# Performance work log

Measured on AMD Instinct MI355X. Metric: run time of the kernel, lower is better.

## Reference

```python
import jax, jax.numpy as jnp
import numpy as np

B, R, P, DP, DR, N, RK = 4, 256, 64, 384, 512, 48, 24


def _ln(x, w, b, eps=1e-5):
    m = x.mean(-1, keepdims=True)
    v = ((x - m) ** 2).mean(-1, keepdims=True)
    return (x - m) / jnp.sqrt(v + eps) * w + b


def _l2norm(x, eps=1e-6):
    return x / jnp.maximum(jnp.linalg.norm(x, axis=-1, keepdims=True), eps)


def setup_inputs() -> dict:
    key = jax.random.key(0)
    ks = jax.random.split(key, 16)
    s = 0.02
    rnd = lambda k, shp: jax.random.normal(k, shp, jnp.float32) * s
    inp = {
        'patch_tokens': jax.random.normal(ks[0], (B, R, P, DP), jnp.float32),
        'patch_mask': jax.random.randint(ks[1], (B, R, P), 0, 2) > 0,
        'near_mask': jax.random.randint(ks[2], (R, R), 0, 2) > 0,
        'far_mask': jax.random.randint(ks[3], (R, R), 0, 2) > 0,
        'local_pos': rnd(ks[4], (1, 1, P, DP)),
        'gate_ln_w': jnp.ones(DP), 'gate_ln_b': jnp.zeros(DP),
        'gate_w1': rnd(ks[5], (DP, DR)), 'gate_b1': jnp.zeros(DR),
        'gate_w2': rnd(ks[6], (DR, 1)), 'gate_b2': jnp.zeros(1),
        'proj_ln1_w': jnp.ones(DP), 'proj_ln1_b': jnp.zeros(DP),
        'proj_w1': rnd(ks[7], (DP, DR)), 'proj_b1': jnp.zeros(DR),
        'proj_w2': rnd(ks[8], (DR, DR)), 'proj_b2': jnp.zeros(DR),
        'proj_ln2_w': jnp.ones(DR), 'proj_ln2_b': jnp.zeros(DR),
        'in_proj_w': rnd(ks[9], (DR, 2 * DR)),
        'x_proj_w': rnd(ks[10], (DR, RK + 2 * N)),
        'dt_w': rnd(ks[11], (RK, DR)),
        'dt_b': jax.random.uniform(ks[12], (DR,), jnp.float32, -4.0, -2.0),
        'A_log': jnp.tile(jnp.log(jnp.arange(1, N + 1, dtype=jnp.float32))[None, :], (DR, 1)),
        'D_param': jnp.ones(DR),
        'out_proj_w': rnd(ks[13], (DR, DR)),
        'scan_ln_w': jnp.ones(DR), 'scan_ln_b': jnp.zeros(DR),
    }
    return inp


def _forward(patch_tokens, patch_mask, near_mask, far_mask, local_pos,
             gate_ln_w, gate_ln_b, gate_w1, gate_b1, gate_w2, gate_b2,
             proj_ln1_w, proj_ln1_b, proj_w1, proj_b1, proj_w2, proj_b2,
             proj_ln2_w, proj_ln2_b, in_proj_w, x_proj_w, dt_w, dt_b,
             A_log, D_param, out_proj_w, scan_ln_w, scan_ln_b):
    # ---- GatedRegionAggregator ----
    x = patch_tokens + local_pos  # [B,R,P,DP]
    g = _ln(x, gate_ln_w, gate_ln_b)
    g = jax.nn.gelu(g @ gate_w1 + gate_b1, approximate=False)
    logits = (g @ gate_w2 + gate_b2)[..., 0]  # [B,R,P]
    logits = jnp.where(patch_mask, logits, jnp.finfo(logits.dtype).min)
    attn = jax.nn.softmax(logits, axis=-1) * patch_mask
    attn = attn / jnp.maximum(attn.sum(-1, keepdims=True), 1e-6)
    pooled = jnp.einsum('brp,brpd->brd', attn, x)  # [B,R,DP]
    p = _ln(pooled, proj_ln1_w, proj_ln1_b)
    p = jax.nn.gelu(p @ proj_w1 + proj_b1, approximate=False)
    p = _ln(p @ proj_w2 + proj_b2, proj_ln2_w, proj_ln2_b)
    p = jnp.nan_to_num(p, nan=0.0, posinf=1.0, neginf=-1.0)
    region = _l2norm(p)  # [B,R,DR]

    # ---- SlowSelectiveScan1D over region sequence (L = R) ----
    xz = region @ in_proj_w  # [B,L,2*DR]
    u, z = jnp.split(xz, 2, axis=-1)
    prm = u @ x_proj_w  # [B,L,RK+2N]
    dt_raw, Bm, Cm = prm[..., :RK], prm[..., RK:RK + N], prm[..., RK + N:]
    delta = jnp.minimum(jax.nn.softplus(dt_raw @ dt_w + dt_b), 10.0)  # [B,L,DR]
    A = -jnp.minimum(jnp.exp(A_log), 1e4)  # [DR,N]
    dA = jnp.exp(jnp.clip(delta[..., None] * A[None, None], -30.0, 30.0))  # [B,L,DR,N]
    dBu = delta[..., None] * Bm[:, :, None, :] * u[..., None]  # [B,L,DR,N]
    log_cumA = jnp.cumsum(jnp.log(jnp.maximum(dA, 1e-38)), axis=1)
    h = jnp.exp(log_cumA) * jnp.cumsum(dBu * jnp.exp(-log_cumA), axis=1)
    y_seq = jnp.einsum('bln,bldn->bld', Cm, h) + D_param * u
    y = (y_seq * jax.nn.silu(z)) @ out_proj_w
    out = _ln(region + jnp.nan_to_num(y, nan=0.0, posinf=1.0, neginf=-1.0),
              scan_ln_w, scan_ln_b)  # [B,R,DR]

    # ---- topology_loss_static ----
    rt = _l2norm(out.astype(jnp.float32))
    sim = jnp.einsum('brd,bsd->brs', rt, rt)  # [B,R,R]
    near = near_mask.astype(sim.dtype)[None]
    far = far_mask.astype(sim.dtype)[None]
    near_loss = ((1.0 - sim) * near).sum() / jnp.maximum(near.sum(), 1.0)
    far_loss = (jax.nn.relu(sim - 0.2) * far).sum() / jnp.maximum(far.sum(), 1.0)
    return out, near_loss + far_loss


def reference(patch_tokens, patch_mask, near_mask, far_mask, local_pos,
              gate_ln_w, gate_ln_b, gate_w1, gate_b1, gate_w2, gate_b2,
              proj_ln1_w, proj_ln1_b, proj_w1, proj_b1, proj_w2, proj_b2,
              proj_ln2_w, proj_ln2_b, in_proj_w, x_proj_w, dt_w, dt_b,
              A_log, D_param, out_proj_w, scan_ln_w, scan_ln_b):
    return _forward(patch_tokens, patch_mask, near_mask, far_mask, local_pos,
                    gate_ln_w, gate_ln_b, gate_w1, gate_b1, gate_w2, gate_b2,
                    proj_ln1_w, proj_ln1_b, proj_w1, proj_b1, proj_w2, proj_b2,
                    proj_ln2_w, proj_ln2_b, in_proj_w, x_proj_w, dt_w, dt_b,
                    A_log, D_param, out_proj_w, scan_ln_w, scan_ln_b)
```

## Files before the change

### kernel.cpp

```cpp
#include <hip/hip_runtime.h>
#include <hip/hip_bf16.h>
#include <math.h>

#define B_ 4
#define R_ 256
#define P_ 64
#define DP_ 384
#define DR_ 512
#define N_ 48
#define RK_ 24
#define MROWS (B_*R_*P_)
#define REGS  (B_*R_)

typedef unsigned short ushort_t;
typedef __attribute__((ext_vector_type(8))) short bf16x8;
typedef __attribute__((ext_vector_type(4))) float f32x4;

#define GLOAD16(g, l) __builtin_amdgcn_global_load_lds( \
    (const __attribute__((address_space(1))) unsigned int*)(g), \
    (__attribute__((address_space(3))) unsigned int*)(l), 16, 0, 0)

#define OFF_PW1  0
#define OFF_PW2  196608
#define OFF_INPW 458752
#define OFF_XPW  983040
#define OFF_DTW  1044480
#define NW_TOT   1056768

__device__ __forceinline__ float us2f(unsigned short u){
  union { unsigned int i; float f; } x; x.i = ((unsigned int)u) << 16; return x.f;
}
__device__ __forceinline__ unsigned short f2us(float f){
  __hip_bfloat16 h = __float2bfloat16(f);
  return *reinterpret_cast<unsigned short*>(&h);
}
__device__ __forceinline__ float gelu_f(float x){
  return 0.5f * x * (1.0f + erff(x * 0.70710678118654752f));
}
__device__ __forceinline__ float wred_sum(float v){
#pragma unroll
  for (int m = 1; m < 64; m <<= 1) v += __shfl_xor(v, m, 64);
  return v;
}
__device__ __forceinline__ void block_sum4(float v[4], float* s){
  int lane = threadIdx.x & 63, wid = threadIdx.x >> 6;
#pragma unroll
  for (int i = 0; i < 4; ++i){
    float x = v[i];
#pragma unroll
    for (int m = 1; m < 64; m <<= 1) x += __shfl_xor(x, m, 64);
    if (lane == 0) s[wid * 4 + i] = x;
  }
  __syncthreads();
  if (threadIdx.x < 4){
    float t = 0.f;
    for (int t2 = 0; t2 < 8; ++t2) t += s[t2 * 4 + threadIdx.x];
    s[32 + threadIdx.x] = t;
  }
  __syncthreads();
#pragma unroll
  for (int i = 0; i < 4; ++i) v[i] = s[32 + i];
  __syncthreads();
}
__device__ __forceinline__ void block_sum2(float& a, float& b, float* s){
  int lane = threadIdx.x & 63, wid = threadIdx.x >> 6;
  float x = a, y = b;
#pragma unroll
  for (int m = 1; m < 64; m <<= 1){ x += __shfl_xor(x, m, 64); y += __shfl_xor(y, m, 64); }
  if (lane == 0){ s[wid * 2] = x; s[wid * 2 + 1] = y; }
  __syncthreads();
  if (threadIdx.x < 2){
    float t = 0.f;
    for (int j = 0; j < 8; ++j) t += s[j * 2 + threadIdx.x];
    s[16 + threadIdx.x] = t;
  }
  __syncthreads();
  a = s[16]; b = s[17];
  __syncthreads();
}

__global__ __launch_bounds__(512) void k_prep(
    const float* __restrict__ gw1, const float* __restrict__ glnw,
    const float* __restrict__ glnb, const float* __restrict__ gb1,
    ushort_t* __restrict__ W1pT, float* __restrict__ s1,
    float* __restrict__ b1p, float* __restrict__ accum){
  __shared__ float pss[8][64], psb[8][64];
  int tid = threadIdx.x, seg = tid >> 6, nl = tid & 63;
  int n = blockIdx.x * 64 + nl;
  if (blockIdx.x == 0 && tid < 4) accum[tid] = 0.f;
  float s = 0.f, sb = 0.f;
  int k0 = seg * 48;
  for (int i = 0; i < 48; ++i){
    int k = k0 + i;
    float w1 = gw1[k * DR_ + n];
    float v = glnw[k] * w1;
    unsigned short vr = f2us(v);
    s  += us2f(vr);
    sb += glnb[k] * w1;
    W1pT[(size_t)n * DP_ + k] = vr;
  }
  pss[seg][nl] = s; psb[seg][nl] = sb;
  __syncthreads();
  if (tid < 64){
    float ts = 0.f, tb = 0.f;
    for (int j = 0; j < 8; ++j){ ts += pss[j][tid]; tb += psb[j][tid]; }
    s1[blockIdx.x * 64 + tid] = ts;
    b1p[blockIdx.x * 64 + tid] = gb1[blockIdx.x * 64 + tid] + tb;
  }
}

__global__ __launch_bounds__(512) void k_cast(
    const float* __restrict__ pw1, const float* __restrict__ pw2,
    const float* __restrict__ inpw, const float* __restrict__ xpw,
    const float* __restrict__ dtw, ushort_t* __restrict__ dst){
  int i = (blockIdx.x * 512 + threadIdx.x) * 4;
  if (i >= NW_TOT) return;
  const float* s; int off;
  if (i < OFF_PW2){ s = pw1; off = OFF_PW1; }
  else if (i < OFF_INPW){ s = pw2; off = OFF_PW2; }
  else if (i < OFF_XPW){ s = inpw; off = OFF_INPW; }
  else if (i < OFF_DTW){ s = xpw; off = OFF_XPW; }
  else { s = dtw; off = OFF_DTW; }
  float4 v = *(const float4*)(s + (i - off));
  ushort_t* d = dst + i;
  d[0] = f2us(v.x); d[1] = f2us(v.y); d[2] = f2us(v.z); d[3] = f2us(v.w);
}

__global__ __launch_bounds__(512) void k_xform(
    const float* __restrict__ pt, const float* __restrict__ lp,
    ushort_t* __restrict__ xb, float* __restrict__ mu, float* __restrict__ rsg){
  int tid = threadIdx.x, w = tid >> 6, lane = tid & 63;
  size_t r = (size_t)blockIdx.x * 8 + w;
  int p = (int)(r & (P_ - 1));
  const float* xr = pt + r * DP_ + lane * 6;
  const float* lr = lp + (size_t)p * DP_ + lane * 6;
  float x[6];
  float s = 0.f, ss = 0.f;
#pragma unroll
  for (int i = 0; i < 6; i += 2){
    float2 a = *(const float2*)(xr + i);
    float2 b = *(const float2*)(lr + i);
    x[i] = a.x + b.x; x[i + 1] = a.y + b.y;
  }
#pragma unroll
  for (int i = 0; i < 6; ++i){ s += x[i]; ss += x[i] * x[i]; }
  s = wred_sum(s); ss = wred_sum(ss);
  if (lane == 0){
    float m = s * (1.f / DP_);
    float var = ss * (1.f / DP_) - m * m;
    mu[r] = m;
    rsg[r] = rsqrtf(var + 1e-5f);
  }
  ushort_t* xw = xb + r * DP_ + lane * 6;
#pragma unroll
  for (int i = 0; i < 6; i += 2){
    ushort2 u2; u2.x = f2us(x[i]); u2.y = f2us(x[i + 1]);
    *(ushort2*)(xw + i) = u2;
  }
}

__global__ __launch_bounds__(512, 4) void k_gate_pool(
    const ushort_t* __restrict__ xb,
    const ushort_t* __restrict__ BT,
    const float* __restrict__ mu, const float* __restrict__ rsg,
    const float* __restrict__ s1, const float* __restrict__ b1p,
    const float* __restrict__ w2, const int* __restrict__ pmask,
    float* __restrict__ pooled){
  __shared__ __align__(16) ushort_t Abuf[2][64 * 64];
  __shared__ float logit_lds[64];
  __shared__ float smu[64], srs[64];
  __shared__ float attn[64];
  int tid = threadIdx.x;
  int lane = tid & 63, w = tid >> 6;
  int t = lane & 15, g = lane >> 4;
  long r0 = (long)blockIdx.x * 64;
  if (tid < 64){
    logit_lds[tid] = 0.f;
    smu[tid] = mu[r0 + tid];
    srs[tid] = rsg[r0 + tid];
  }

  f32x4 acc[4][4];
#pragma unroll
  for (int m = 0; m < 4; ++m)
#pragma unroll
    for (int n = 0; n < 4; ++n) acc[m][n] = (f32x4){0.f, 0.f, 0.f, 0.f};

  int arow8 = (w << 3) + (lane >> 3);
  int akc = lane & 7;
  const ushort_t* asrc0 = xb + (size_t)(r0 + arow8) * DP_ + ((akc ^ (arow8 & 7)) << 3);
  ushort_t* adst0 = Abuf[0] + (w << 9);
  ushort_t* adst1 = Abuf[1] + (w << 9);

  GLOAD16(asrc0, adst0);
  __syncthreads();

  for (int kt = 0; kt < 6; ++kt){
    if (kt < 5) GLOAD16(asrc0 + (kt + 1) * 64, (kt & 1) ? adst0 : adst1);
    const ushort_t* cbuf = (kt & 1) ? Abuf[1] : Abuf[0];
    bf16x8 bfr[2][4];
#pragma unroll
    for (int kk = 0; kk < 2; ++kk)
#pragma unroll
      for (int n = 0; n < 4; ++n){
        int rowb = w * 64 + n * 16 + t;
        bfr[kk][n] = *(const bf16x8*)(BT + (size_t)rowb * DP_ + kt * 64 + (kk * 4 + g) * 8);
      }
#pragma unroll
    for (int kk = 0; kk < 2; ++kk){
      int ch = kk * 4 + g;
      bf16x8 af[4];
#pragma unroll
      for (int m = 0; m < 4; ++m){
        int row = m * 16 + t;
        af[m] = *(const bf16x8*)(cbuf + row * 64 + ((ch ^ (row & 7)) << 3));
      }
#pragma unroll
      for (int m = 0; m < 4; ++m)
#pragma unroll
        for (int n = 0; n < 4; ++n)
          acc[m][n] = __builtin_amdgcn_mfma_f32_16x16x32_bf16(af[m], bfr[kk][n], acc[m][n], 0, 0, 0);
    }
    __syncthreads();
  }

  float w2c[4], s1c[4], b1c[4];
#pragma unroll
  for (int n = 0; n < 4; ++n){
    int c = w * 64 + n * 16 + t;
    w2c[n] = w2[c]; s1c[n] = s1[c]; b1c[n] = b1p[c];
  }
#pragma unroll
  for (int m = 0; m < 4; ++m){
#pragma unroll
    for (int j = 0; j < 4; ++j){
      int rl = m * 16 + g * 4 + j;
      float mur = smu[rl], rs = srs[rl];
      float part = 0.f;
#pragma unroll
      for (int n = 0; n < 4; ++n){
        float gp = rs * acc[m][n][j] - mur * rs * s1c[n] + b1c[n];
        part += gelu_f(gp) * w2c[n];
      }
#pragma unroll
      for (int msk = 1; msk < 16; msk <<= 1) part += __shfl_xor(part, msk, 64);
      if (t == 0) atomicAdd(&logit_lds[rl], part);
    }
  }
  __syncthreads();

  if (tid < 64){
    int mk = pmask[r0 + tid];
    float lv = logit_lds[tid];
    float lm = mk ? lv : -3.4e38f;
    float M = lm;
#pragma unroll
    for (int m2 = 1; m2 < 64; m2 <<= 1) M = fmaxf(M, __shfl_xor(M, m2, 64));
    float e = mk ? __expf(lv - M) : 0.f;
    float S = e;
#pragma unroll
    for (int m2 = 1; m2 < 64; m2 <<= 1) S += __shfl_xor(S, m2, 64);
    float a = (S > 0.f) ? e / S : 0.f;
    float S2 = a;
#pragma unroll
    for (int m2 = 1; m2 < 64; m2 <<= 1) S2 += __shfl_xor(S2, m2, 64);
    attn[tid] = a / fmaxf(S2, 1e-6f);
  }
  __syncthreads();

  if (tid < DP_){
    float accp = 0.f;
#pragma unroll 4
    for (int p = 0; p < P_; ++p)
      accp += attn[p] * us2f(xb[(size_t)(r0 + p) * DP_ + tid]);
    pooled[(long)blockIdx.x * DP_ + tid] = accp;
  }
}

__global__ __launch_bounds__(512, 4) void k_region(
    const float* __restrict__ pooled,
    const float* __restrict__ ln1w, const float* __restrict__ ln1b,
    const ushort_t* __restrict__ wblob, const float* __restrict__ pb1,
    const float* __restrict__ pb2,
    const float* __restrict__ ln2w, const float* __restrict__ ln2b,
    const float* __restrict__ dtb,
    float* __restrict__ region, float* __restrict__ uT, float* __restrict__ zT,
    float* __restrict__ deltaT, float* __restrict__ BmT, float* __restrict__ CmT){
  const ushort_t* pw1b  = wblob + OFF_PW1;
  const ushort_t* pw2b  = wblob + OFF_PW2;
  const ushort_t* inpwb = wblob + OFF_INPW;
  const ushort_t* xpwb  = wblob + OFF_XPW;
  const ushort_t* dtwb  = wblob + OFF_DTW;
  __shared__ float xr[2][DP_];
  __shared__ float p1[2][DR_];
  __shared__ float rg[2][DR_];
  __shared__ float us[2][DR_];
  __shared__ float ps[4][2][128];
  __shared__ float prm[2][RK_ + 2 * N_];
  __shared__ float red[24];
  int tid = threadIdx.x;
  int r0 = blockIdx.x * 2;
  for (int i = tid; i < 2 * DP_; i += 512) xr[i / DP_][i % DP_] = pooled[(long)r0 * DP_ + i];
  __syncthreads();
  float v0 = (tid < DP_) ? xr[0][tid] : 0.f;
  float v1 = (tid < DP_) ? xr[1][tid] : 0.f;
  float s0 = v0, s1v = v1;
  block_sum2(s0, s1v, red);
  float dv0 = (tid < DP_) ? (v0 - s0 * (1.f / DP_)) : 0.f;
  float dv1 = (tid < DP_) ? (v1 - s1v * (1.f / DP_)) : 0.f;
  float q0 = dv0 * dv0, q1 = dv1 * dv1;
  block_sum2(q0, q1, red);
  if (tid < DP_){
    float lw = ln1w[tid], lb = ln1b[tid];
    xr[0][tid] = dv0 * rsqrtf(q0 * (1.f / DP_) + 1e-5f) * lw + lb;
    xr[1][tid] = dv1 * rsqrtf(q1 * (1.f / DP_) + 1e-5f) * lw + lb;
  }
  __syncthreads();
  {
    float pb = pb1[tid];
    float a0 = pb, a1 = pb;
    for (int k0 = 0; k0 < DP_; k0 += 16){
      ushort_t wv[16];
#pragma unroll
      for (int j = 0; j < 16; ++j) wv[j] = pw1b[(k0 + j) * DR_ + tid];
#pragma unroll
      for (int j = 0; j < 16; ++j){
        float wf = us2f(wv[j]);
        a0 = fmaf(xr[0][k0 + j], wf, a0);
        a1 = fmaf(xr[1][k0 + j], wf, a1);
      }
    }
    p1[0][tid] = gelu_f(a0); p1[1][tid] = gelu_f(a1);
  }
  __syncthreads();
  float qq0, qq1;
  {
    float pb = pb2[tid];
    float a0 = pb, a1 = pb;
    for (int k0 = 0; k0 < DR_; k0 += 16){
      ushort_t wv[16];
#pragma unroll
      for (int j = 0; j < 16; ++j) wv[j] = pw2b[(k0 + j) * DR_ + tid];
#pragma unroll
      for (int j = 0; j < 16; ++j){
        float wf = us2f(wv[j]);
        a0 = fmaf(p1[0][k0 + j], wf, a0);
        a1 = fmaf(p1[1][k0 + j], wf, a1);
      }
    }
    qq0 = a0; qq1 = a1;
  }
  {
    float m0 = qq0, m1 = qq1;
    block_sum2(m0, m1, red);
    float d0 = qq0 - m0 * (1.f / DR_), d1 = qq1 - m1 * (1.f / DR_);
    float w0 = d0 * d0, w1 = d1 * d1;
    block_sum2(w0, w1, red);
    float lw = ln2w[tid], lb = ln2b[tid];
    float o0 = d0 * rsqrtf(w0 * (1.f / DR_) + 1e-5f) * lw + lb;
    float o1 = d1 * rsqrtf(w1 * (1.f / DR_) + 1e-5f) * lw + lb;
    if (isnan(o0)) o0 = 0.f; else if (isinf(o0)) o0 = (o0 > 0.f) ? 1.f : -1.f;
    if (isnan(o1)) o1 = 0.f; else if (isinf(o1)) o1 = (o1 > 0.f) ? 1.f : -1.f;
    float n0 = o0 * o0, n1 = o1 * o1;
    block_sum2(n0, n1, red);
    float r0v = o0 / fmaxf(sqrtf(n0), 1e-6f);
    float r1v = o1 / fmaxf(sqrtf(n1), 1e-6f);
    rg[0][tid] = r0v; rg[1][tid] = r1v;
    region[(long)r0 * DR_ + tid] = r0v;
    region[(long)(r0 + 1) * DR_ + tid] = r1v;
  }
  __syncthreads();
  {
    float ua0 = 0.f, ua1 = 0.f, zb0 = 0.f, zb1 = 0.f;
    for (int k0 = 0; k0 < DR_; k0 += 8){
      ushort_t w1v[8], w2v[8];
#pragma unroll
      for (int j = 0; j < 8; ++j){
        w1v[j] = inpwb[(k0 + j) * 1024 + tid];
        w2v[j] = inpwb[(k0 + j) * 1024 + tid + 512];
      }
#pragma unroll
      for (int j = 0; j < 8; ++j){
        float x0 = rg[0][k0 + j], x1 = rg[1][k0 + j];
        float wa = us2f(w1v[j]), wb = us2f(w2v[j]);
        ua0 = fmaf(x0, wa, ua0); ua1 = fmaf(x1, wa, ua1);
        zb0 = fmaf(x0, wb, zb0); zb1 = fmaf(x1, wb, zb1);
      }
    }
    us[0][tid] = ua0; us[1][tid] = ua1;
    uT[(long)tid * REGS + r0] = ua0;
    uT[(long)tid * REGS + r0 + 1] = ua1;
    zT[(long)tid * REGS + r0] = zb0;
    zT[(long)tid * REGS + r0 + 1] = zb1;
  }
  __syncthreads();
  {
    int sseg = tid >> 7, c = tid & 127;
    float pr0 = 0.f, pr1 = 0.f;
    if (c < RK_ + 2 * N_){
      int kb = sseg * 128;
      for (int k0 = kb; k0 < kb + 128; k0 += 16){
        ushort_t wv[16];
#pragma unroll
        for (int j = 0; j < 16; ++j) wv[j] = xpwb[(k0 + j) * (RK_ + 2 * N_) + c];
#pragma unroll
        for (int j = 0; j < 16; ++j){
          float wf = us2f(wv[j]);
          pr0 = fmaf(us[0][k0 + j], wf, pr0);
          pr1 = fmaf(us[1][k0 + j], wf, pr1);
        }
      }
    }
    ps[sseg][0][c] = pr0; ps[sseg][1][c] = pr1;
  }
  __syncthreads();
  if (tid < 256){
    int rr2 = tid >> 7, cc = tid & 127;
    if (cc < RK_ + 2 * N_)
      prm[rr2][cc] = ps[0][rr2][cc] + ps[1][rr2][cc] + ps[2][rr2][cc] + ps[3][rr2][cc];
  }
  __syncthreads();
#pragma unroll
  for (int r = 0; r < 2; ++r){
    float aa = dtb[tid];
#pragma unroll
    for (int j = 0; j < RK_; ++j) aa = fmaf(prm[r][j], us2f(dtwb[j * DR_ + tid]), aa);
    float sp = (aa > 20.f) ? aa : log1pf(expf(aa));
    deltaT[(long)tid * REGS + r0 + r] = fminf(sp, 10.f);
  }
  if (tid < N_){
#pragma unroll
    for (int r = 0; r < 2; ++r){
      BmT[(long)tid * REGS + r0 + r] = prm[r][RK_ + tid];
      CmT[(long)tid * REGS + r0 + r] = prm[r][RK_ + N_ + tid];
    }
  }
}

__global__ __launch_bounds__(256) void k_scan(
    const float* __restrict__ deltaT, const float* __restrict__ uT,
    const float* __restrict__ zT, const float* __restrict__ BmT,
    const float* __restrict__ CmT, const float* __restrict__ alog,
    const float* __restrict__ Dp, float* __restrict__ ys){
  __shared__ float sAn[N_];
  __shared__ float sA[N_][4];
  __shared__ float sB[N_][4];
  int tid = threadIdx.x, lane = tid & 63, w = tid >> 6;
  int ch = blockIdx.x;
  int b = ch >> 9, d = ch & (DR_ - 1);
  if (tid < N_) sAn[tid] = -fminf(__expf(alog[d * N_ + tid]), 10000.f);
  long col = (long)b * R_ + tid;
  float dl = deltaT[(long)d * REGS + col];
  float uu = uT[(long)d * REGS + col];
  float zz = zT[(long)d * REGS + col];
  float Dd = Dp[d];
  float part = 0.f;
  __syncthreads();
  for (int nc = 0; nc < 6; ++nc){
    float bmv[8], cmv[8];
#pragma unroll
    for (int j = 0; j < 8; ++j){
      bmv[j] = BmT[(long)(nc * 8 + j) * REGS + col];
      cmv[j] = CmT[(long)(nc * 8 + j) * REGS + col];
    }
    float aA[8], aB[8];
#pragma unroll
    for (int j = 0; j < 8; ++j){
      int n = nc * 8 + j;
      float cc = fminf(fmaxf(dl * sAn[n], -30.f), 30.f);
      float a = exp2f(cc * 1.44269504f);
      float bv = dl * bmv[j] * uu;
#pragma unroll
      for (int s = 1; s < 64; s <<= 1){
        float a_sh = __shfl_up(a, (unsigned)s, 64);
        float b_sh = __shfl_up(bv, (unsigned)s, 64);
        float nb = fmaf(a, b_sh, bv);
        float na = a * a_sh;
        if (lane >= s){ bv = nb; a = na; }
      }
      aA[j] = a; aB[j] = bv;
      if (lane == 63){ sA[n][w] = a; sB[n][w] = bv; }
    }
    __syncthreads();
#pragma unroll
    for (int j = 0; j < 8; ++j){
      int n = nc * 8 + j;
      float hin = 0.f;
#pragma unroll
      for (int tt = 0; tt < 3; ++tt){
        if (tt < w) hin = sA[n][tt] * hin + sB[n][tt];
      }
      float h = fmaf(aA[j], hin, aB[j]);
      part = fmaf(cmv[j], h, part);
    }
    if (nc < 5) __syncthreads();
  }
  float yv = part + Dd * uu;
  float sz = zz / (1.f + __expf(-zz));
  ys[col * DR_ + d] = yv * sz;
}

__global__ __launch_bounds__(512) void k_out(
    const float* __restrict__ ys, const float* __restrict__ W,
    const float* __restrict__ region, const float* __restrict__ lnw,
    const float* __restrict__ lnb, float* __restrict__ outp,
    float* __restrict__ rt){
  __shared__ float yr[4][DR_];
  __shared__ float red[40];
  int tid = threadIdx.x;
  int r0 = blockIdx.x * 4;
  for (int i = tid; i < 4 * DR_; i += 512) yr[i >> 9][i & 511] = ys[(long)r0 * DR_ + i];
  __syncthreads();
  float y[4] = {0,0,0,0};
  for (int k0 = 0; k0 < DR_; k0 += 8){
    float wv[8];
#pragma unroll
    for (int j = 0; j < 8; ++j) wv[j] = W[(k0 + j) * DR_ + tid];
#pragma unroll
    for (int j = 0; j < 8; ++j){
#pragma unroll
      for (int i = 0; i < 4; ++i) y[i] = fmaf(yr[i][k0 + j], wv[j], y[i]);
    }
  }
  float v[4], t4[4];
#pragma unroll
  for (int i = 0; i < 4; ++i){
    if (isnan(y[i])) y[i] = 0.f; else if (isinf(y[i])) y[i] = (y[i] > 0.f) ? 1.f : -1.f;
    v[i] = region[(long)(r0 + i) * DR_ + tid] + y[i];
    t4[i] = v[i];
  }
  block_sum4(t4, red);
  float dv[4];
#pragma unroll
  for (int i = 0; i < 4; ++i){ dv[i] = v[i] - t4[i] * (1.f / DR_); t4[i] = dv[i] * dv[i]; }
  block_sum4(t4, red);
  float o[4];
  float lw = lnw[tid], lb = lnb[tid];
#pragma unroll
  for (int i = 0; i < 4; ++i){
    o[i] = dv[i] * rsqrtf(t4[i] * (1.f / DR_) + 1e-5f) * lw + lb;
    outp[(long)(r0 + i) * DR_ + tid] = o[i];
    t4[i] = o[i] * o[i];
  }
  block_sum4(t4, red);
#pragma unroll
  for (int i = 0; i < 4; ++i)
    rt[(long)(r0 + i) * DR_ + tid] = o[i] / fmaxf(sqrtf(t4[i]), 1e-6f);
}

__global__ __launch_bounds__(512) void k_loss(
    const float* __restrict__ rt, const int* __restrict__ nearm,
    const int* __restrict__ farm, float* __restrict__ accum){
  __shared__ __align__(16) float ar[4][DR_];
  __shared__ float ps[2][4][256];
  __shared__ float wsum[8][4];
  int blk = blockIdx.x, tid = threadIdx.x;
  int b = blk >> 6, q0 = (blk & 63) * 4;
  const float* rtb = rt + (long)b * R_ * DR_;
  for (int i = tid; i < 4 * DR_; i += 512) ar[i >> 9][i & 511] = rtb[(long)q0 * DR_ + i];
  __syncthreads();
  int s = tid & 255, h = tid >> 8;
  const float* rsrow = rtb + (long)s * DR_ + h * 256;
  float dq[4] = {0.f, 0.f, 0.f, 0.f};
  for (int k = 0; k < 256; k += 4){
    float4 yv = *(const float4*)(rsrow + k);
#pragma unroll
    for (int q = 0; q < 4; ++q){
      float4 x = *(const float4*)(&ar[q][h * 256 + k]);
      dq[q] += x.x * yv.x + x.y * yv.y + x.z * yv.z + x.w * yv.w;
    }
  }
#pragma unroll
  for (int q = 0; q < 4; ++q) ps[h][q][s] = dq[q];
  __syncthreads();
  float nl = 0.f, fl = 0.f, nc = 0.f, fc = 0.f;
  if (tid < 256){
#pragma unroll
    for (int q = 0; q < 4; ++q){
      float dot = ps[0][q][tid] + ps[1][q][tid];
      int nm = nearm[(q0 + q) * R_ + tid], fm = farm[(q0 + q) * R_ + tid];
      if (nm){ nl += 1.f - dot; if (b == 0) nc += 1.f; }
      if (fm){ fl += fmaxf(dot - 0.2f, 0.f); if (b == 0) fc += 1.f; }
    }
  }
  nl = wred_sum(nl); fl = wred_sum(fl); nc = wred_sum(nc); fc = wred_sum(fc);
  int w = tid >> 6, lane = tid & 63;
  if (lane == 0){ wsum[w][0] = nl; wsum[w][1] = fl; wsum[w][2] = nc; wsum[w][3] = fc; }
  __syncthreads();
  if (tid == 0){
    float a0 = 0, a1 = 0, a2 = 0, a3 = 0;
    for (int i = 0; i < 8; i++){ a0 += wsum[i][0]; a1 += wsum[i][1]; a2 += wsum[i][2]; a3 += wsum[i][3]; }
    atomicAdd(&accum[0], a0); atomicAdd(&accum[1], a1);
    if (b == 0){ atomicAdd(&accum[2], a2); atomicAdd(&accum[3], a3); }
  }
}

__global__ void k_final(const float* __restrict__ accum, float* __restrict__ outp){
  if (threadIdx.x == 0){
    float loss = accum[0] / fmaxf(accum[2], 1.f) + accum[1] / fmaxf(accum[3], 1.f);
    outp[REGS * DR_] = loss;
  }
}

extern "C" void kernel_launch(void* const* d_in, const int* in_sizes, int n_in,
                              void* d_out, int out_size, void* d_ws, size_t ws_size,
                              hipStream_t stream){
  const float* pt    = (const float*)d_in[0];
  const int*   pmask = (const int*)d_in[1];
  const int*   nearm = (const int*)d_in[2];
  const int*   farm  = (const int*)d_in[3];
  const float* lp    = (const float*)d_in[4];
  const float* glnw  = (const float*)d_in[5];
  const float* glnb  = (const float*)d_in[6];
  const float* gw1   = (const float*)d_in[7];
  const float* gb1   = (const float*)d_in[8];
  const float* gw2   = (const float*)d_in[9];
  const float* pln1w = (const float*)d_in[11];
  const float* pln1b = (const float*)d_in[12];
  const float* pw1   = (const float*)d_in[13];
  const float* pb1   = (const float*)d_in[14];
  const float* pw2   = (const float*)d_in[15];
  const float* pb2   = (const float*)d_in[16];
  const float* pln2w = (const float*)d_in[17];
  const float* pln2b = (const float*)d_in[18];
  const float* inpw  = (const float*)d_in[19];
  const float* xpw   = (const float*)d_in[20];
  const float* dtw   = (const float*)d_in[21];
  const float* dtb   = (const float*)d_in[22];
  const float* alog  = (const float*)d_in[23];
  const float* dpar  = (const float*)d_in[24];
  const float* opw   = (const float*)d_in[25];
  const float* slnw  = (const float*)d_in[26];
  const float* slnb  = (const float*)d_in[27];

  char* ws = (char*)d_ws;
  size_t off = 0;
  auto alloc = [&](size_t bytes){ size_t o = off; off += (bytes + 255) & ~(size_t)255; return o; };
  ushort_t* W1pT  = (ushort_t*)(ws + alloc((size_t)DR_ * DP_ * 2));
  float* s1     = (float*)(ws + alloc(DR_ * 4));
  float* b1p    = (float*)(ws + alloc(DR_ * 4));
  ushort_t* wblob = (ushort_t*)(ws + alloc((size_t)NW_TOT * 2));
  ushort_t* xb  = (ushort_t*)(ws + alloc((size_t)MROWS * DP_ * 2));
  float* mu     = (float*)(ws + alloc((size_t)MROWS * 4));
  float* rsg    = (float*)(ws + alloc((size_t)MROWS * 4));
  float* pooled = (float*)(ws + alloc((size_t)REGS * DP_ * 4));
  float* region = (float*)(ws + alloc((size_t)REGS * DR_ * 4));
  float* uT     = (float*)(ws + alloc((size_t)REGS * DR_ * 4));
  float* zT     = (float*)(ws + alloc((size_t)REGS * DR_ * 4));
  float* deltaT = (float*)(ws + alloc((size_t)REGS * DR_ * 4));
  float* BmT    = (float*)(ws + alloc((size_t)REGS * N_ * 4));
  float* CmT    = (float*)(ws + alloc((size_t)REGS * N_ * 4));
  float* ys     = (float*)(ws + alloc((size_t)REGS * DR_ * 4));
  float* rt     = (float*)(ws + alloc((size_t)REGS * DR_ * 4));
  float* accum  = (float*)(ws + alloc(4 * 4));

  float* outp = (float*)d_out;

  k_prep<<<dim3(8), dim3(512), 0, stream>>>(gw1, glnw, glnb, gb1, W1pT, s1, b1p, accum);
  k_cast<<<dim3((NW_TOT / 4 + 511) / 512), dim3(512), 0, stream>>>(pw1, pw2, inpw, xpw, dtw, wblob);
  k_xform<<<dim3(MROWS / 8), dim3(512), 0, stream>>>(pt, lp, xb, mu, rsg);
  k_gate_pool<<<dim3(REGS), dim3(512), 0, stream>>>(xb, W1pT, mu, rsg, s1, b1p, gw2, pmask, pooled);
  k_region<<<dim3(REGS / 2), dim3(512), 0, stream>>>(pooled, pln1w, pln1b, wblob, pb1, pb2, pln2w, pln2b,
                                                     dtb, region, uT, zT, deltaT, BmT, CmT);
  k_scan<<<dim3(B_ * DR_), dim3(256), 0, stream>>>(deltaT, uT, zT, BmT, CmT, alog, dpar, ys);
  k_out<<<dim3(REGS / 4), dim3(512), 0, stream>>>(ys, opw, region, slnw, slnb, outp, rt);
  k_loss<<<dim3(REGS / 4), dim3(512), 0, stream>>>(rt, nearm, farm, accum);
  k_final<<<dim3(1), dim3(64), 0, stream>>>(accum, outp);
}
```

Before: 322.1 us.

## Split gate and pooling kernels, prefetch full A tile, vectorize pooling

The gate kernel now loads all six K-slices of the 64x384 bf16 A tile into LDS up front with a single barrier, replacing the double-buffered loop that synchronised on every iteration. Launch bounds drop to 2 blocks per CU to make room for the larger LDS buffer. Attention softmax and weighted pooling move into a separate kernel that reads logits from global memory and uses 16-byte vector loads with a partial-sum reduction across 8 patch groups. This cuts per-iteration barriers and the strided scalar pooling loads, at the cost of an extra launch, a logits round-trip through global memory, and lower occupancy in the gate kernel.

After: 335.7 us. 1.04x slower.

```diff
diff --git a/kernel.cpp b/kernel.cpp
--- a/kernel.cpp
+++ b/kernel.cpp
@@ -159,17 +159,15 @@
   }
 }
 
-__global__ __launch_bounds__(512, 4) void k_gate_pool(
+__global__ __launch_bounds__(512, 2) void k_gate(
     const ushort_t* __restrict__ xb,
     const ushort_t* __restrict__ BT,
     const float* __restrict__ mu, const float* __restrict__ rsg,
     const float* __restrict__ s1, const float* __restrict__ b1p,
-    const float* __restrict__ w2, const int* __restrict__ pmask,
-    float* __restrict__ pooled){
-  __shared__ __align__(16) ushort_t Abuf[2][64 * 64];
+    const float* __restrict__ w2, float* __restrict__ logits){
+  __shared__ __align__(16) ushort_t Abuf[6][64 * 64];
   __shared__ float logit_lds[64];
   __shared__ float smu[64], srs[64];
-  __shared__ float attn[64];
   int tid = threadIdx.x;
   int lane = tid & 63, w = tid >> 6;
   int t = lane & 15, g = lane >> 4;
@@ -189,15 +187,13 @@
   int arow8 = (w << 3) + (lane >> 3);
   int akc = lane & 7;
   const ushort_t* asrc0 = xb + (size_t)(r0 + arow8) * DP_ + ((akc ^ (arow8 & 7)) << 3);
-  ushort_t* adst0 = Abuf[0] + (w << 9);
-  ushort_t* adst1 = Abuf[1] + (w << 9);
-
-  GLOAD16(asrc0, adst0);
-  __syncthreads();
-
+#pragma unroll
+  for (int kt = 0; kt < 6; ++kt)
+    GLOAD16(asrc0 + kt * 64, Abuf[kt] + (w << 9));
+  __syncthreads();
+
+#pragma unroll
   for (int kt = 0; kt < 6; ++kt){
-    if (kt < 5) GLOAD16(asrc0 + (kt + 1) * 64, (kt & 1) ? adst0 : adst1);
-    const ushort_t* cbuf = (kt & 1) ? Abuf[1] : Abuf[0];
     bf16x8 bfr[2][4];
 #pragma unroll
     for (int kk = 0; kk < 2; ++kk)
@@ -213,7 +209,7 @@
 #pragma unroll
       for (int m = 0; m < 4; ++m){
         int row = m * 16 + t;
-        af[m] = *(const bf16x8*)(cbuf + row * 64 + ((ch ^ (row & 7)) << 3));
+        af[m] = *(const bf16x8*)(Abuf[kt] + row * 64 + ((ch ^ (row & 7)) << 3));
       }
 #pragma unroll
       for (int m = 0; m < 4; ++m)
@@ -221,7 +217,6 @@
         for (int n = 0; n < 4; ++n)
           acc[m][n] = __builtin_amdgcn_mfma_f32_16x16x32_bf16(af[m], bfr[kk][n], acc[m][n], 0, 0, 0);
     }
-    __syncthreads();
   }
 
   float w2c[4], s1c[4], b1c[4];
@@ -248,10 +243,19 @@
     }
   }
   __syncthreads();
-
+  if (tid < 64) logits[r0 + tid] = logit_lds[tid];
+}
+
+__global__ __launch_bounds__(512) void k_pool(
+    const ushort_t* __restrict__ xb, const float* __restrict__ logits,
+    const int* __restrict__ pmask, float* __restrict__ pooled){
+  __shared__ float attn[64];
+  __shared__ float part[8][DP_];
+  int tid = threadIdx.x;
+  long r0 = (long)blockIdx.x * 64;
   if (tid < 64){
     int mk = pmask[r0 + tid];
-    float lv = logit_lds[tid];
+    float lv = logits[r0 + tid];
     float lm = mk ? lv : -3.4e38f;
     float M = lm;
 #pragma unroll
@@ -267,13 +271,26 @@
     attn[tid] = a / fmaxf(S2, 1e-6f);
   }
   __syncthreads();
-
+  if (tid < 384){
+    int pg = tid / 48, c = tid % 48;
+    float acc[8] = {0,0,0,0,0,0,0,0};
+#pragma unroll
+    for (int i = 0; i < 8; ++i){
+      int p = pg + i * 8;
+      bf16x8 v = *(const bf16x8*)(xb + (size_t)(r0 + p) * DP_ + c * 8);
+      float ap = attn[p];
+#pragma unroll
+      for (int j = 0; j < 8; ++j) acc[j] = fmaf(ap, us2f((unsigned short)v[j]), acc[j]);
+    }
+#pragma unroll
+    for (int j = 0; j < 8; ++j) part[pg][c * 8 + j] = acc[j];
+  }
+  __syncthreads();
   if (tid < DP_){
-    float accp = 0.f;
-#pragma unroll 4
-    for (int p = 0; p < P_; ++p)
-      accp += attn[p] * us2f(xb[(size_t)(r0 + p) * DP_ + tid]);
-    pooled[(long)blockIdx.x * DP_ + tid] = accp;
+    float s = 0.f;
+#pragma unroll
+    for (int g2 = 0; g2 < 8; ++g2) s += part[g2][tid];
+    pooled[(long)blockIdx.x * DP_ + tid] = s;
   }
 }
 
@@ -643,6 +660,7 @@
   ushort_t* xb  = (ushort_t*)(ws + alloc((size_t)MROWS * DP_ * 2));
   float* mu     = (float*)(ws + alloc((size_t)MROWS * 4));
   float* rsg    = (float*)(ws + alloc((size_t)MROWS * 4));
+  float* logits = (float*)(ws + alloc((size_t)MROWS * 4));
   float* pooled = (float*)(ws + alloc((size_t)REGS * DP_ * 4));
   float* region = (float*)(ws + alloc((size_t)REGS * DR_ * 4));
   float* uT     = (float*)(ws + alloc((size_t)REGS * DR_ * 4));
@@ -659,7 +677,8 @@
   k_prep<<<dim3(8), dim3(512), 0, stream>>>(gw1, glnw, glnb, gb1, W1pT, s1, b1p, accum);
   k_cast<<<dim3((NW_TOT / 4 + 511) / 512), dim3(512), 0, stream>>>(pw1, pw2, inpw, xpw, dtw, wblob);
   k_xform<<<dim3(MROWS / 8), dim3(512), 0, stream>>>(pt, lp, xb, mu, rsg);
-  k_gate_pool<<<dim3(REGS), dim3(512), 0, stream>>>(xb, W1pT, mu, rsg, s1, b1p, gw2, pmask, pooled);
+  k_gate<<<dim3(REGS), dim3(512), 0, stream>>>(xb, W1pT, mu, rsg, s1, b1p, gw2, logits);
+  k_pool<<<dim3(REGS), dim3(512), 0, stream>>>(xb, logits, pmask, pooled);
   k_region<<<dim3(REGS / 2), dim3(512), 0, stream>>>(pooled, pln1w, pln1b, wblob, pb1, pb2, pln2w, pln2b,
                                                      dtb, region, uT, zT, deltaT, BmT, CmT);
   k_scan<<<dim3(B_ * DR_), dim3(256), 0, stream>>>(deltaT, uT, zT, BmT, CmT, alog, dpar, ys);
```
